# Performance work log

Measured on AMD Instinct MI355X. Metric: run time of the kernel, lower is better.

Reference implementation:

```python
import jax, jax.numpy as jnp
import numpy as np

B, C, E, TARGET = 8, 256, 18000, 4500


def setup_inputs() -> dict:
    key = jax.random.key(0)
    k1, k2 = jax.random.split(key)
    fe = jax.random.normal(k1, (B, C, E), dtype=jnp.float32)
    # group_ids[b, e] = index of the pooled output edge that original edge e
    # was merged into by the union-find during edge collapse.
    group_ids = jax.random.randint(k2, (B, E), 0, TARGET, dtype=jnp.int64)
    return {"fe": fe, "group_ids": group_ids, "target": TARGET}


def reference(fe, group_ids, target):
    # MeshUnion.rebuild_features: out feature of each surviving edge group =
    # mean of features of all original edges merged into that group.
    b, c, e = fe.shape
    # flatten (batch, group) into one segment id so a single segment_sum handles all meshes
    flat_ids = (jnp.arange(b, dtype=group_ids.dtype)[:, None] * target + group_ids).reshape(-1)  # [B*E]
    feats = fe.transpose(0, 2, 1).reshape(b * e, c)  # [B*E, C]
    sums = jax.ops.segment_sum(feats, flat_ids, num_segments=b * target)          # [B*T, C]
    counts = jax.ops.segment_sum(jnp.ones((b * e,), fe.dtype), flat_ids,
                                 num_segments=b * target)                          # [B*T]
    out = sums / jnp.maximum(counts, 1.0)[:, None]
    return out.reshape(b, target, c).transpose(0, 2, 1)  # [B, C, target]
```

## Files before the change

kernel.cpp:

```cpp
#include <hip/hip_runtime.h>

#define BB 8
#define CC 256
#define EE 18000
#define TT 4500
#define BT (BB * TT)
#define BE (BB * EE)
#define W  18
#define SS 19
#define NT 1024
#define PW (NT * SS)


__global__ void zero_counts_kernel(int* __restrict__ counts) {
    int i = blockIdx.x * blockDim.x + threadIdx.x;
    if (i < BT) counts[i] = 0;
}

__global__ void count_kernel(const int* __restrict__ gid, int* __restrict__ counts) {
    int i = blockIdx.x * blockDim.x + threadIdx.x;
    if (i < BE) {
        int b = i / EE;
        atomicAdd(&counts[b * TT + gid[i]], 1);
    }
}

__global__ __launch_bounds__(1024) void scan_kernel(const int* __restrict__ counts,
                                                    int* __restrict__ cursor,
                                                    uint2* __restrict__ tab) {
    __shared__ int part[1024];
    const int b = blockIdx.x;
    const int t = threadIdx.x;
    const int CHUNK = 5;
    int lo = t * CHUNK; if (lo > TT) lo = TT;
    int hi = lo + CHUNK; if (hi > TT) hi = TT;
    int s = 0;
    for (int i = lo; i < hi; ++i) s += counts[b * TT + i];
    part[t] = s;
    __syncthreads();
    for (int d = 1; d < 1024; d <<= 1) {
        int v = (t >= d) ? part[t - d] : 0;
        __syncthreads();
        part[t] += v;
        __syncthreads();
    }
    int run = part[t] - s;
    for (int i = lo; i < hi; ++i) {
        int cnt = counts[b * TT + i];
        cursor[b * TT + i] = b * EE + run;
        int en = run + cnt;
        unsigned int qa = cnt ? (unsigned int)((en - 1) + (en - 1) / W + 1) : 0u;
        unsigned int qb = run ? (unsigned int)((run - 1) + (run - 1) / W + 1) : 0u;
        float inv = cnt ? 1.0f / (float)cnt : 0.0f;
        tab[b * TT + i] = make_uint2(qa | (qb << 16), __float_as_uint(inv));
        run = en;
    }
}

__global__ void scatter_kernel(const int* __restrict__ gid,
                               int* __restrict__ cursor,
                               unsigned short* __restrict__ prank16) {
    int i = blockIdx.x * blockDim.x + threadIdx.x;
    if (i < BE) {
        int b = i / EE;
        int p = atomicAdd(&cursor[b * TT + gid[i]], 1) - b * EE;
        prank16[i] = (unsigned short)(p + p / W);
    }
}


__global__ __launch_bounds__(1024, 8) void pool_kernel(const float* __restrict__ fe,
                                                       const unsigned short* __restrict__ prank16,
                                                       const uint2* __restrict__ tab,
                                                       float* __restrict__ out) {
    __shared__ float vals[PW];
    __shared__ float wsum[16];
    const int b   = blockIdx.x >> 8;
    const int c   = blockIdx.x & 255;
    const int tid = threadIdx.x;
    const int wv  = tid >> 6;
    const int ln  = tid & 63;

    const float4*  fe4 = (const float4*)(fe + (size_t)(b * CC + c) * EE);
    const ushort4* rk4 = (const ushort4*)(prank16 + (size_t)b * EE);
#pragma unroll
    for (int i = 0; i < 5; ++i) {
        int idx = tid + (i << 10);
        if (idx < EE / 4) {
            float4  v = fe4[idx];
            ushort4 r = rk4[idx];
            vals[r.x] = v.x;
            vals[r.y] = v.y;
            vals[r.z] = v.z;
            vals[r.w] = v.w;
        }
    }
    __syncthreads();

    const int base = SS * tid;
    float v[W];
    float s0 = 0.0f, s1 = 0.0f;
#pragma unroll
    for (int k = 0; k < 9; ++k)  { v[k] = vals[base + k]; s0 += v[k]; }
#pragma unroll
    for (int k = 9; k < 18; ++k) { v[k] = vals[base + k]; s1 += v[k]; }
    const float sum = s0 + s1;

    float sc = sum;
#pragma unroll
    for (int d = 1; d < 64; d <<= 1) {
        float o = __shfl_up(sc, d, 64);
        if (ln >= d) sc += o;
    }
    if (ln == 63) wsum[wv] = sc;
    __syncthreads();

    float cross = 0.0f;
#pragma unroll
    for (int j = 0; j < 16; ++j) {
        float tw = wsum[j];
        if (j < wv) cross += tw;
    }

    float run0 = cross + (sc - sum);
    float run1 = run0 + s0;
#pragma unroll
    for (int k = 0; k < 9; ++k)  { run0 += v[k]; vals[base + k] = run0; }
#pragma unroll
    for (int k = 9; k < 18; ++k) { run1 += v[k]; vals[base + k] = run1; }
    __syncthreads();

    const uint2* tb   = tab + b * TT;
    float*       outb = out + (size_t)(b * CC + c) * TT;
#pragma unroll
    for (int k = 0; k < 5; ++k) {
        int g = tid + (k << 10);
        if (g < TT) {
            uint2 q = tb[g];
            unsigned int a  = q.x & 0xffffu;
            unsigned int bq = q.x >> 16;
            float Pa = a  ? vals[a - 1]  : 0.0f;
            float Pb = bq ? vals[bq - 1] : 0.0f;
            outb[g] = (Pa - Pb) * __uint_as_float(q.y);
        }
    }
}

extern "C" void kernel_launch(void* const* d_in, const int* in_sizes, int n_in,
                              void* d_out, int out_size, void* d_ws, size_t ws_size,
                              hipStream_t stream) {
    const float* fe  = (const float*)d_in[0];
    const int*   gid = (const int*)d_in[1];
    float*       out = (float*)d_out;

    int*            counts  = (int*)d_ws;
    int*            cursor  = counts + BT;
    uint2*          tab     = (uint2*)(cursor + BT);
    unsigned short* prank16 = (unsigned short*)(tab + BT);

    zero_counts_kernel<<<(BT + 255) / 256, 256, 0, stream>>>(counts);
    count_kernel<<<(BE + 255) / 256, 256, 0, stream>>>(gid, counts);
    scan_kernel<<<BB, 1024, 0, stream>>>(counts, cursor, tab);
    scatter_kernel<<<(BE + 255) / 256, 256, 0, stream>>>(gid, cursor, prank16);
    pool_kernel<<<BB * CC, 1024, 0, stream>>>(fe, prank16, tab, out);
}
```

Measured before the change: 65.88 us.

## Use unpadded shared prefix layout with float4 LDS access and 512-thread pool blocks

Measured after the change: 70.31 us. 6.7% more time.

```diff
diff --git a/kernel.cpp b/kernel.cpp
--- a/kernel.cpp
+++ b/kernel.cpp
@@ -6,10 +6,9 @@
 #define TT 4500
 #define BT (BB * TT)
 #define BE (BB * EE)
-#define W  18
-#define SS 19
-#define NT 1024
-#define PW (NT * SS)
+#define NT 512
+#define W  36
+#define PW (NT * W)
 
 
 __global__ void zero_counts_kernel(int* __restrict__ counts) {
@@ -49,10 +48,9 @@
         int cnt = counts[b * TT + i];
         cursor[b * TT + i] = b * EE + run;
         int en = run + cnt;
-        unsigned int qa = cnt ? (unsigned int)((en - 1) + (en - 1) / W + 1) : 0u;
-        unsigned int qb = run ? (unsigned int)((run - 1) + (run - 1) / W + 1) : 0u;
         float inv = cnt ? 1.0f / (float)cnt : 0.0f;
-        tab[b * TT + i] = make_uint2(qa | (qb << 16), __float_as_uint(inv));
+        tab[b * TT + i] = make_uint2((unsigned)run | ((unsigned)en << 16),
+                                     __float_as_uint(inv));
         run = en;
     }
 }
@@ -64,17 +62,17 @@
     if (i < BE) {
         int b = i / EE;
         int p = atomicAdd(&cursor[b * TT + gid[i]], 1) - b * EE;
-        prank16[i] = (unsigned short)(p + p / W);
+        prank16[i] = (unsigned short)p;
     }
 }
 
 
-__global__ __launch_bounds__(1024, 8) void pool_kernel(const float* __restrict__ fe,
-                                                       const unsigned short* __restrict__ prank16,
-                                                       const uint2* __restrict__ tab,
-                                                       float* __restrict__ out) {
+__global__ __launch_bounds__(512, 4) void pool_kernel(const float* __restrict__ fe,
+                                                      const unsigned short* __restrict__ prank16,
+                                                      const uint2* __restrict__ tab,
+                                                      float* __restrict__ out) {
     __shared__ float vals[PW];
-    __shared__ float wsum[16];
+    __shared__ float wsum[8];
     const int b   = blockIdx.x >> 8;
     const int c   = blockIdx.x & 255;
     const int tid = threadIdx.x;
@@ -84,8 +82,8 @@
     const float4*  fe4 = (const float4*)(fe + (size_t)(b * CC + c) * EE);
     const ushort4* rk4 = (const ushort4*)(prank16 + (size_t)b * EE);
 #pragma unroll
-    for (int i = 0; i < 5; ++i) {
-        int idx = tid + (i << 10);
+    for (int i = 0; i < 9; ++i) {
+        int idx = tid + (i << 9);
         if (idx < EE / 4) {
             float4  v = fe4[idx];
             ushort4 r = rk4[idx];
@@ -97,14 +95,22 @@
     }
     __syncthreads();
 
-    const int base = SS * tid;
-    float v[W];
-    float s0 = 0.0f, s1 = 0.0f;
+    const int base = W * tid;
+    float4 pv[9];
+    float  csum[9];
 #pragma unroll
-    for (int k = 0; k < 9; ++k)  { v[k] = vals[base + k]; s0 += v[k]; }
-#pragma unroll
-    for (int k = 9; k < 18; ++k) { v[k] = vals[base + k]; s1 += v[k]; }
-    const float sum = s0 + s1;
+    for (int k = 0; k < 9; ++k) {
+        float4 v = *reinterpret_cast<float4*>(&vals[base + (k << 2)]);
+        float p0 = v.x;
+        float p1 = p0 + v.y;
+        float p2 = p1 + v.z;
+        float p3 = p2 + v.w;
+        pv[k] = make_float4(p0, p1, p2, p3);
+        csum[k] = p3;
+    }
+    float t01 = csum[0] + csum[1], t23 = csum[2] + csum[3];
+    float t45 = csum[4] + csum[5], t67 = csum[6] + csum[7];
+    const float sum = ((t01 + t23) + (t45 + t67)) + csum[8];
 
     float sc = sum;
 #pragma unroll
@@ -117,30 +123,32 @@
 
     float cross = 0.0f;
 #pragma unroll
-    for (int j = 0; j < 16; ++j) {
+    for (int j = 0; j < 8; ++j) {
         float tw = wsum[j];
         if (j < wv) cross += tw;
     }
 
-    float run0 = cross + (sc - sum);
-    float run1 = run0 + s0;
+    float off = cross + (sc - sum);
 #pragma unroll
-    for (int k = 0; k < 9; ++k)  { run0 += v[k]; vals[base + k] = run0; }
-#pragma unroll
-    for (int k = 9; k < 18; ++k) { run1 += v[k]; vals[base + k] = run1; }
+    for (int k = 0; k < 9; ++k) {
+        float4 p = pv[k];
+        float4 o = make_float4(p.x + off, p.y + off, p.z + off, p.w + off);
+        *reinterpret_cast<float4*>(&vals[base + (k << 2)]) = o;
+        off += csum[k];
+    }
     __syncthreads();
 
     const uint2* tb   = tab + b * TT;
     float*       outb = out + (size_t)(b * CC + c) * TT;
 #pragma unroll
-    for (int k = 0; k < 5; ++k) {
-        int g = tid + (k << 10);
+    for (int k = 0; k < 9; ++k) {
+        int g = tid + (k << 9);
         if (g < TT) {
             uint2 q = tb[g];
-            unsigned int a  = q.x & 0xffffu;
-            unsigned int bq = q.x >> 16;
-            float Pa = a  ? vals[a - 1]  : 0.0f;
-            float Pb = bq ? vals[bq - 1] : 0.0f;
+            unsigned int st = q.x & 0xffffu;
+            unsigned int en = q.x >> 16;
+            float Pa = en ? vals[en - 1] : 0.0f;
+            float Pb = st ? vals[st - 1] : 0.0f;
             outb[g] = (Pa - Pb) * __uint_as_float(q.y);
         }
     }
@@ -162,5 +170,5 @@
     count_kernel<<<(BE + 255) / 256, 256, 0, stream>>>(gid, counts);
     scan_kernel<<<BB, 1024, 0, stream>>>(counts, cursor, tab);
     scatter_kernel<<<(BE + 255) / 256, 256, 0, stream>>>(gid, cursor, prank16);
-    pool_kernel<<<BB * CC, 1024, 0, stream>>>(fe, prank16, tab, out);
+    pool_kernel<<<BB * CC, 512, 0, stream>>>(fe, prank16, tab, out);
 }
```
